# Kernel optimization log

Measured on AMD Instinct MI355X. Metric: run time of the kernel, lower is better.

The kernel has to match this reference:

```python
import jax, jax.numpy as jnp
import numpy as np

D_MODEL = 768
N_HEADS = 12
D_K = D_MODEL // N_HEADS


def setup_inputs() -> dict:
    key = jax.random.key(0)
    k_x, k_wqkv, k_bqkv, k_wo, k_bo = jax.random.split(key, 5)
    s = 1.0 / np.sqrt(D_MODEL)
    return {
        "x": jax.random.normal(k_x, (2, 4096, D_MODEL), dtype=jnp.float32),
        "w_qkv": jax.random.uniform(k_wqkv, (D_MODEL, 3 * D_MODEL), jnp.float32, -s, s),
        "b_qkv": jax.random.uniform(k_bqkv, (3 * D_MODEL,), jnp.float32, -s, s),
        "w_out": jax.random.uniform(k_wo, (D_MODEL, D_MODEL), jnp.float32, -s, s),
        "b_out": jax.random.uniform(k_bo, (D_MODEL,), jnp.float32, -s, s),
    }


def reference(x, w_qkv, b_qkv, w_out, b_out):
    B, S, E = x.shape
    qkv = x @ w_qkv + b_qkv                                  # [B,S,3E]
    qkv = qkv.reshape(B, S, 3, N_HEADS, D_K)
    qkv = jnp.transpose(qkv, (2, 0, 3, 1, 4))                # [3,B,H,S,Dk]
    q, k, v = qkv[0], qkv[1], qkv[2]
    scores = jnp.einsum("bhsd,bhtd->bhst", q, k) / jnp.sqrt(jnp.float32(D_K))
    attn = jax.nn.softmax(scores, axis=-1)                   # [B,H,S,S]
    ctx = jnp.einsum("bhst,bhtd->bhsd", attn, v)             # [B,H,S,Dk]
    ctx = jnp.transpose(ctx, (0, 2, 1, 3)).reshape(B, S, E)  # [B,S,E]
    return ctx @ w_out + b_out
```

## Files before the change

kernel.cpp:

```cpp
#include <hip/hip_runtime.h>

typedef short short8 __attribute__((ext_vector_type(8)));
typedef float f32x4 __attribute__((ext_vector_type(4)));
typedef float f32x16 __attribute__((ext_vector_type(16)));
typedef unsigned short u16;
typedef unsigned int u32;

__device__ __forceinline__ u16 f2bf(float f) {
  u32 u = __float_as_uint(f);
  u32 r = u + 0x7fffu + ((u >> 16) & 1u);
  return (u16)(r >> 16);
}

__device__ __forceinline__ u32 cvtpk(float lo, float hi) {
  u32 r;
  asm("v_cvt_pk_bf16_f32 %0, %1, %2" : "=v"(r) : "v"(lo), "v"(hi));
  return r;
}

__device__ __forceinline__ void async_copy16(u16* lds_dst, const u16* gsrc) {
  __builtin_amdgcn_global_load_lds(
      (const __attribute__((address_space(1))) u32*)gsrc,
      (__attribute__((address_space(3))) u32*)lds_dst, 16, 0, 0);
}

__global__ void cvt_f32_bf16(const float4* __restrict__ in, uint2* __restrict__ out, int n4) {
  int i = blockIdx.x * blockDim.x + threadIdx.x;
  if (i >= n4) return;
  float4 v = in[i];
  uint2 o;
  o.x = (u32)f2bf(v.x) | ((u32)f2bf(v.y) << 16);
  o.y = (u32)f2bf(v.z) | ((u32)f2bf(v.w) << 16);
  out[i] = o;
}

__global__ __launch_bounds__(256) void cvt_transpose_w(
    const float* __restrict__ W, u16* __restrict__ WT, int K, int N) {
  __shared__ float tl[32 * 33];
  int n0 = blockIdx.x * 32, k0 = blockIdx.y * 32;
  int tx = threadIdx.x & 31, ty = threadIdx.x >> 5;
#pragma unroll
  for (int j = 0; j < 4; ++j)
    tl[(ty + j * 8) * 33 + tx] = W[(size_t)(k0 + ty + j * 8) * N + n0 + tx];
  __syncthreads();
#pragma unroll
  for (int j = 0; j < 4; ++j)
    WT[(size_t)(n0 + ty + j * 8) * K + k0 + tx] = f2bf(tl[tx * 33 + ty + j * 8]);
}

__global__ __launch_bounds__(256) void transpose_v(
    const u16* __restrict__ V, u16* __restrict__ VT) {
  __shared__ u16 tb[64 * 66];
  const int tid = threadIdx.x;
  const int bh = blockIdx.y;
  const int t0 = blockIdx.x * 64;
  const u16* Vb = V + (size_t)bh * 4096 * 64;
  u16* VTb = VT + (size_t)bh * 64 * 4096;
#pragma unroll
  for (int it = 0; it < 2; ++it) {
    int cid = it * 256 + tid;
    int row = cid >> 3, c = cid & 7;
    short8 v = *(const short8*)&Vb[(size_t)(t0 + row) * 64 + c * 8];
#pragma unroll
    for (int i = 0; i < 8; ++i) tb[row * 66 + c * 8 + i] = (u16)v[i];
  }
  __syncthreads();
#pragma unroll
  for (int it = 0; it < 2; ++it) {
    int pid = it * 256 + tid;
    int c2 = pid & 7, d = pid >> 3;
    short8 o;
#pragma unroll
    for (int i = 0; i < 8; ++i) o[i] = (short)tb[(c2 * 8 + i) * 66 + d];
    *(short8*)&VTb[(size_t)d * 4096 + t0 + c2 * 8] = o;
  }
}

#define BM 128
#define BN 128
#define BKG 64

template <int EPI>
__global__ __launch_bounds__(256, 2) void gemm_bf16(
    const u16* __restrict__ A, const u16* __restrict__ Bt,
    const float* __restrict__ bias, int M, int N, int K,
    u16* __restrict__ q_out, u16* __restrict__ k_out, u16* __restrict__ v_out,
    float* __restrict__ c_out) {
  __shared__ u16 lA[BM * BKG];
  __shared__ u16 lB[BN * BKG];
  const int tid = threadIdx.x;
  const int lane = tid & 63;
  const int wid = tid >> 6;
  const int r = lane & 15, hi = lane >> 4;
  const int m0 = blockIdx.y * BM;
  const int n0 = blockIdx.x * BN;
  const int wm = (wid >> 1) * 64;
  const int wn = (wid & 1) * 64;

  f32x4 acc[4][4];
#pragma unroll
  for (int i = 0; i < 4; ++i)
#pragma unroll
    for (int j = 0; j < 4; ++j) acc[i][j] = f32x4{0.f, 0.f, 0.f, 0.f};

  for (int k0 = 0; k0 < K; k0 += BKG) {
#pragma unroll
    for (int j = 0; j < 4; ++j) {
      int cid = j * 256 + tid;
      int row = cid >> 3, c = cid & 7;
      async_copy16(&lA[cid * 8], &A[(size_t)(m0 + row) * K + k0 + c * 8]);
    }
#pragma unroll
    for (int j = 0; j < 4; ++j) {
      int cid = j * 256 + tid;
      int row = cid >> 3, c = cid & 7;
      async_copy16(&lB[cid * 8], &Bt[(size_t)(n0 + row) * K + k0 + c * 8]);
    }
    __syncthreads();
#pragma unroll
    for (int kk = 0; kk < 2; ++kk) {
      short8 af[4], bfr[4];
#pragma unroll
      for (int i = 0; i < 4; ++i)
        af[i] = *(const short8*)&lA[(wm + i * 16 + r) * BKG + kk * 32 + hi * 8];
#pragma unroll
      for (int i = 0; i < 4; ++i)
        bfr[i] = *(const short8*)&lB[(wn + i * 16 + r) * BKG + kk * 32 + hi * 8];
#pragma unroll
      for (int i = 0; i < 4; ++i)
#pragma unroll
        for (int j = 0; j < 4; ++j)
          acc[i][j] = __builtin_amdgcn_mfma_f32_16x16x32_bf16(af[i], bfr[j], acc[i][j], 0, 0, 0);
    }
    __syncthreads();
  }

#pragma unroll
  for (int i = 0; i < 4; ++i) {
#pragma unroll
    for (int j = 0; j < 4; ++j) {
      int gn = n0 + wn + j * 16 + r;
      float bv = bias[gn];
#pragma unroll
      for (int q = 0; q < 4; ++q) {
        int gm = m0 + wm + i * 16 + hi * 4 + q;
        float v = acc[i][j][q] + bv;
        if (EPI == 0) {
          int part = gn / 768;
          int rem = gn - part * 768;
          int h = rem >> 6, d = rem & 63;
          int b = gm >> 12, s = gm & 4095;
          size_t off = (((size_t)(b * 12 + h) * 4096) + s) * 64 + d;
          if (part == 0) q_out[off] = f2bf(v * 0.18033688011112042f);
          else if (part == 1) k_out[off] = f2bf(v);
          else v_out[off] = f2bf(v);
        } else {
          c_out[(size_t)gm * N + gn] = v;
        }
      }
    }
  }
}

__global__ __launch_bounds__(256, 3) void attn_fwd(
    const u16* __restrict__ Qg, const u16* __restrict__ Kg,
    const u16* __restrict__ VTg, u16* __restrict__ ctxg) {
  __shared__ u16 lK[2][64 * 64];
  __shared__ u16 lV[2][64 * 64];
  const int tid = threadIdx.x;
  const int lane = tid & 63, wid = tid >> 6;
  const int q32 = lane & 31, half = lane >> 5;
  const int bh = blockIdx.y;
  const int s0 = blockIdx.x * 128;
  const int qrow = s0 + wid * 32 + q32;
  const u16* Qb = Qg + (size_t)bh * 4096 * 64;
  const u16* Kb = Kg + (size_t)bh * 4096 * 64;
  const u16* Vb = VTg + (size_t)bh * 64 * 4096;

  short8 qf[4];
#pragma unroll
  for (int dc = 0; dc < 4; ++dc)
    qf[dc] = *(const short8*)&Qb[(size_t)qrow * 64 + dc * 16 + half * 8];

  f32x16 acc0, acc1;
#pragma unroll
  for (int i = 0; i < 16; ++i) { acc0[i] = 0.f; acc1[i] = 0.f; }
  float l_run = 0.f;

#define STAGE(buf, t0_)                                                      \
  do {                                                                       \
    _Pragma("unroll") for (int j = 0; j < 2; ++j) {                          \
      int cid = j * 256 + tid;                                               \
      int row = cid >> 3, c = cid & 7, cs = c ^ (row & 7);                   \
      async_copy16(&lK[buf][cid * 8], &Kb[(size_t)((t0_) + row) * 64 + cs * 8]); \
    }                                                                        \
    _Pragma("unroll") for (int j = 0; j < 2; ++j) {                          \
      int cid = j * 256 + tid;                                               \
      int row = cid >> 3, c = cid & 7, cs = c ^ (row & 7);                   \
      async_copy16(&lV[buf][cid * 8], &Vb[(size_t)row * 4096 + (t0_) + cs * 8]); \
    }                                                                        \
  } while (0)

  STAGE(0, 0);
  int cur = 0;

  for (int t0 = 0; t0 < 4096; t0 += 64) {
    __syncthreads();
    if (t0 + 64 < 4096) STAGE(cur ^ 1, t0 + 64);

    const char* lKc = (const char*)lK[cur];
    const char* lVc = (const char*)lV[cur];

    f32x16 sA, sB;
#pragma unroll
    for (int i = 0; i < 16; ++i) { sA[i] = 0.f; sB[i] = 0.f; }
    const int xorq = (q32 & 7);
    __builtin_amdgcn_s_setprio(1);
#pragma unroll
    for (int dc = 0; dc < 4; ++dc) {
      int ch = dc * 2 + half;
      short8 kA = *(const short8*)(lKc + q32 * 128 + ((ch ^ xorq) << 4));
      short8 kB = *(const short8*)(lKc + (32 + q32) * 128 + ((ch ^ xorq) << 4));
      sA = __builtin_amdgcn_mfma_f32_32x32x16_bf16(kA, qf[dc], sA, 0, 0, 0);
      sB = __builtin_amdgcn_mfma_f32_32x32x16_bf16(kB, qf[dc], sB, 0, 0, 0);
    }
    __builtin_amdgcn_s_setprio(0);

    float pA[16], pB[16];
#pragma unroll
    for (int i = 0; i < 16; ++i) pA[i] = exp2f(sA[i]);
#pragma unroll
    for (int i = 0; i < 16; ++i) pB[i] = exp2f(sB[i]);
    {
      float ps0 = 0.f, ps1 = 0.f, ps2 = 0.f, ps3 = 0.f;
#pragma unroll
      for (int i = 0; i < 16; i += 4) {
        ps0 += pA[i]; ps1 += pA[i + 1]; ps2 += pA[i + 2]; ps3 += pA[i + 3];
        ps0 += pB[i]; ps1 += pB[i + 1]; ps2 += pB[i + 2]; ps3 += pB[i + 3];
      }
      l_run += (ps0 + ps1) + (ps2 + ps3);
    }

    u32 w0[8], w1[8];
#pragma unroll
    for (int g = 0; g < 4; ++g) {
      w0[g] = cvtpk(pA[4 * g + 0], pA[4 * g + 1]);
      w1[g] = cvtpk(pA[4 * g + 2], pA[4 * g + 3]);
      w0[4 + g] = cvtpk(pB[4 * g + 0], pB[4 * g + 1]);
      w1[4 + g] = cvtpk(pB[4 * g + 2], pB[4 * g + 3]);
    }

    __builtin_amdgcn_s_setprio(1);
#pragma unroll
    for (int ks = 0; ks < 4; ++ks) {
      u32 x0 = w0[2 * ks], y0 = w0[2 * ks + 1];
      u32 x1 = w1[2 * ks], y1 = w1[2 * ks + 1];
      asm("v_permlane32_swap_b32 %0, %1" : "+v"(x0), "+v"(y0));
      asm("v_permlane32_swap_b32 %0, %1" : "+v"(x1), "+v"(y1));
      union { u32 u[4]; short8 s; } pa;
      pa.u[0] = x0; pa.u[1] = x1; pa.u[2] = y0; pa.u[3] = y1;
      int ch = ks * 2 + half;
      {
        int d = q32;
        short8 vf = *(const short8*)(lVc + d * 128 + ((ch ^ (d & 7)) << 4));
        acc0 = __builtin_amdgcn_mfma_f32_32x32x16_bf16(pa.s, vf, acc0, 0, 0, 0);
      }
      {
        int d = 32 + q32;
        short8 vf = *(const short8*)(lVc + d * 128 + ((ch ^ (d & 7)) << 4));
        acc1 = __builtin_amdgcn_mfma_f32_32x32x16_bf16(pa.s, vf, acc1, 0, 0, 0);
      }
    }
    __builtin_amdgcn_s_setprio(0);
    cur ^= 1;
  }

  float l_tot = l_run + __shfl_xor(l_run, 32);
  float inv = 1.f / l_tot;
  int b = bh / 12, h = bh - b * 12;
#pragma unroll
  for (int reg = 0; reg < 16; ++reg) {
    int row = (reg & 3) + 8 * (reg >> 2) + 4 * half;
    float iv = __shfl(inv, row);
    size_t base = ((size_t)b * 4096 + s0 + wid * 32 + row) * 768 + h * 64;
    ctxg[base + q32] = f2bf(acc0[reg] * iv);
    ctxg[base + 32 + q32] = f2bf(acc1[reg] * iv);
  }
}

extern "C" void kernel_launch(void* const* d_in, const int* in_sizes, int n_in,
                              void* d_out, int out_size, void* d_ws, size_t ws_size,
                              hipStream_t stream) {
  const float* x = (const float*)d_in[0];
  const float* w_qkv = (const float*)d_in[1];
  const float* b_qkv = (const float*)d_in[2];
  const float* w_out = (const float*)d_in[3];
  const float* b_out = (const float*)d_in[4];
  float* out = (float*)d_out;

  char* ws = (char*)d_ws;
  const size_t SZ_X = (size_t)8192 * 768 * 2;
  const size_t SZ_WQ = (size_t)2304 * 768 * 2;
  const size_t SZ_WO = (size_t)768 * 768 * 2;
  const size_t SZ_HSD = (size_t)24 * 4096 * 64 * 2;
  u16* xb = (u16*)ws;     ws += SZ_X;
  u16* wqkvT = (u16*)ws;  ws += SZ_WQ;
  u16* woutT = (u16*)ws;  ws += SZ_WO;
  u16* Qb = (u16*)ws;     ws += SZ_HSD;
  u16* Kb = (u16*)ws;     ws += SZ_HSD;
  u16* Vb = (u16*)ws;     ws += SZ_HSD;
  u16* VTb = (u16*)ws;    ws += SZ_HSD;
  u16* ctxb = (u16*)ws;   ws += SZ_X;

  cvt_f32_bf16<<<dim3(6144), dim3(256), 0, stream>>>(
      (const float4*)x, (uint2*)xb, 8192 * 768 / 4);
  cvt_transpose_w<<<dim3(72, 24), dim3(256), 0, stream>>>(w_qkv, wqkvT, 768, 2304);
  cvt_transpose_w<<<dim3(24, 24), dim3(256), 0, stream>>>(w_out, woutT, 768, 768);
  gemm_bf16<0><<<dim3(18, 64), dim3(256), 0, stream>>>(
      xb, wqkvT, b_qkv, 8192, 2304, 768, Qb, Kb, Vb, (float*)nullptr);
  transpose_v<<<dim3(64, 24), dim3(256), 0, stream>>>(Vb, VTb);
  attn_fwd<<<dim3(32, 24), dim3(256), 0, stream>>>(Qb, Kb, VTb, ctxb);
  gemm_bf16<1><<<dim3(6, 64), dim3(256), 0, stream>>>(
      ctxb, woutT, b_out, 8192, 768, 768, (u16*)nullptr, (u16*)nullptr, (u16*)nullptr, out);
}
```

Measured before the change: 255.4 us.

## Software-pipeline attention loop with triple-buffered K/V and QK-ahead overlap

Restructures the attention main loop so each iteration computes the QK scores of the next tile while running softmax and PV on the current tile. K/V go from double to triple buffering in LDS, with prefetch two tiles ahead and the loop unrolled by three so buffer indices are compile-time constants. The first QK MFMA now starts from a zero accumulator instead of zero-filled score registers. The aim is to hide exp/convert latency behind matrix-core work and give loads more time to land. In exchange it uses more LDS per block and keeps more score registers live, which may pressure occupancy.

Result: slower. 452.5 us (+77.2%).

```diff
diff --git a/kernel.cpp b/kernel.cpp
--- a/kernel.cpp
+++ b/kernel.cpp
@@ -165,8 +165,8 @@
 __global__ __launch_bounds__(256, 3) void attn_fwd(
     const u16* __restrict__ Qg, const u16* __restrict__ Kg,
     const u16* __restrict__ VTg, u16* __restrict__ ctxg) {
-  __shared__ u16 lK[2][64 * 64];
-  __shared__ u16 lV[2][64 * 64];
+  __shared__ u16 lK[3][64 * 64];
+  __shared__ u16 lV[3][64 * 64];
   const int tid = threadIdx.x;
   const int lane = tid & 63, wid = tid >> 6;
   const int q32 = lane & 31, half = lane >> 5;
@@ -176,103 +176,126 @@
   const u16* Qb = Qg + (size_t)bh * 4096 * 64;
   const u16* Kb = Kg + (size_t)bh * 4096 * 64;
   const u16* Vb = VTg + (size_t)bh * 64 * 4096;
+  const int xorq = q32 & 7;
 
   short8 qf[4];
 #pragma unroll
   for (int dc = 0; dc < 4; ++dc)
     qf[dc] = *(const short8*)&Qb[(size_t)qrow * 64 + dc * 16 + half * 8];
 
+  f32x16 zc;
+#pragma unroll
+  for (int i = 0; i < 16; ++i) zc[i] = 0.f;
+
   f32x16 acc0, acc1;
 #pragma unroll
   for (int i = 0; i < 16; ++i) { acc0[i] = 0.f; acc1[i] = 0.f; }
   float l_run = 0.f;
-
-#define STAGE(buf, t0_)                                                      \
+  f32x16 sA, sB;
+
+#define STAGE(BUF, TI)                                                       \
   do {                                                                       \
     _Pragma("unroll") for (int j = 0; j < 2; ++j) {                          \
       int cid = j * 256 + tid;                                               \
       int row = cid >> 3, c = cid & 7, cs = c ^ (row & 7);                   \
-      async_copy16(&lK[buf][cid * 8], &Kb[(size_t)((t0_) + row) * 64 + cs * 8]); \
+      async_copy16(&lK[BUF][cid * 8],                                        \
+                   &Kb[(size_t)((TI) * 64 + row) * 64 + cs * 8]);            \
     }                                                                        \
     _Pragma("unroll") for (int j = 0; j < 2; ++j) {                          \
       int cid = j * 256 + tid;                                               \
       int row = cid >> 3, c = cid & 7, cs = c ^ (row & 7);                   \
-      async_copy16(&lV[buf][cid * 8], &Vb[(size_t)row * 4096 + (t0_) + cs * 8]); \
+      async_copy16(&lV[BUF][cid * 8],                                        \
+                   &Vb[(size_t)row * 4096 + (TI) * 64 + cs * 8]);            \
     }                                                                        \
   } while (0)
 
+#define QK_TILE(BUF)                                                          \
+  {                                                                           \
+    const char* lKc = (const char*)lK[BUF];                                   \
+    {                                                                         \
+      short8 kA = *(const short8*)(lKc + q32 * 128 + ((half ^ xorq) << 4));   \
+      short8 kB = *(const short8*)(lKc + (32 + q32) * 128 + ((half ^ xorq) << 4)); \
+      sA = __builtin_amdgcn_mfma_f32_32x32x16_bf16(kA, qf[0], zc, 0, 0, 0);   \
+      sB = __builtin_amdgcn_mfma_f32_32x32x16_bf16(kB, qf[0], zc, 0, 0, 0);   \
+    }                                                                         \
+    _Pragma("unroll") for (int dc = 1; dc < 4; ++dc) {                        \
+      int ch = dc * 2 + half;                                                 \
+      short8 kA = *(const short8*)(lKc + q32 * 128 + ((ch ^ xorq) << 4));     \
+      short8 kB = *(const short8*)(lKc + (32 + q32) * 128 + ((ch ^ xorq) << 4)); \
+      sA = __builtin_amdgcn_mfma_f32_32x32x16_bf16(kA, qf[dc], sA, 0, 0, 0);  \
+      sB = __builtin_amdgcn_mfma_f32_32x32x16_bf16(kB, qf[dc], sB, 0, 0, 0);  \
+    }                                                                         \
+  }
+
+#define SM_TILE()                                                             \
+  u32 w0[8], w1[8];                                                           \
+  {                                                                           \
+    float ps0 = 0.f, ps1 = 0.f, ps2 = 0.f, ps3 = 0.f;                        \
+    _Pragma("unroll") for (int g = 0; g < 4; ++g) {                           \
+      float a0 = exp2f(sA[4 * g + 0]), a1 = exp2f(sA[4 * g + 1]);             \
+      float a2 = exp2f(sA[4 * g + 2]), a3 = exp2f(sA[4 * g + 3]);             \
+      w0[g] = cvtpk(a0, a1); w1[g] = cvtpk(a2, a3);                           \
+      ps0 += a0; ps1 += a1; ps2 += a2; ps3 += a3;                             \
+      float b0 = exp2f(sB[4 * g + 0]), b1 = exp2f(sB[4 * g + 1]);             \
+      float b2 = exp2f(sB[4 * g + 2]), b3 = exp2f(sB[4 * g + 3]);             \
+      w0[4 + g] = cvtpk(b0, b1); w1[4 + g] = cvtpk(b2, b3);                   \
+      ps0 += b0; ps1 += b1; ps2 += b2; ps3 += b3;                             \
+    }                                                                         \
+    l_run += (ps0 + ps1) + (ps2 + ps3);                                       \
+  }
+
+#define PV_TILE(BUF)                                                          \
+  {                                                                           \
+    const char* lVc = (const char*)lV[BUF];                                   \
+    __builtin_amdgcn_s_setprio(1);                                            \
+    _Pragma("unroll") for (int ks = 0; ks < 4; ++ks) {                        \
+      u32 x0 = w0[2 * ks], y0 = w0[2 * ks + 1];                               \
+      u32 x1 = w1[2 * ks], y1 = w1[2 * ks + 1];                               \
+      asm("v_permlane32_swap_b32 %0, %1" : "+v"(x0), "+v"(y0));               \
+      asm("v_permlane32_swap_b32 %0, %1" : "+v"(x1), "+v"(y1));               \
+      union { u32 u[4]; short8 s; } pa;                                       \
+      pa.u[0] = x0; pa.u[1] = x1; pa.u[2] = y0; pa.u[3] = y1;                 \
+      int ch = ks * 2 + half;                                                 \
+      {                                                                       \
+        int d = q32;                                                          \
+        short8 vf = *(const short8*)(lVc + d * 128 + ((ch ^ (d & 7)) << 4));  \
+        acc0 = __builtin_amdgcn_mfma_f32_32x32x16_bf16(pa.s, vf, acc0, 0, 0, 0); \
+      }                                                                       \
+      {                                                                       \
+        int d = 32 + q32;                                                     \
+        short8 vf = *(const short8*)(lVc + d * 128 + ((ch ^ (d & 7)) << 4));  \
+        acc1 = __builtin_amdgcn_mfma_f32_32x32x16_bf16(pa.s, vf, acc1, 0, 0, 0); \
+      }                                                                       \
+    }                                                                         \
+    __builtin_amdgcn_s_setprio(0);                                            \
+  }
+
+#define BODY(B0, B1, B2, T, STG)                                              \
+  {                                                                           \
+    __syncthreads();                                                          \
+    if (STG) STAGE(B2, (T) + 2);                                              \
+    SM_TILE();                                                                \
+    QK_TILE(B1);                                                              \
+    PV_TILE(B0);                                                              \
+  }
+
   STAGE(0, 0);
-  int cur = 0;
-
-  for (int t0 = 0; t0 < 4096; t0 += 64) {
+  STAGE(1, 1);
+  __syncthreads();
+  QK_TILE(0);
+
+  for (int t3 = 0; t3 < 60; t3 += 3) {
+    BODY(0, 1, 2, t3, true);
+    BODY(1, 2, 0, t3 + 1, true);
+    BODY(2, 0, 1, t3 + 2, true);
+  }
+  BODY(0, 1, 2, 60, true);
+  BODY(1, 2, 0, 61, true);
+  BODY(2, 0, 1, 62, false);
+  {
     __syncthreads();
-    if (t0 + 64 < 4096) STAGE(cur ^ 1, t0 + 64);
-
-    const char* lKc = (const char*)lK[cur];
-    const char* lVc = (const char*)lV[cur];
-
-    f32x16 sA, sB;
-#pragma unroll
-    for (int i = 0; i < 16; ++i) { sA[i] = 0.f; sB[i] = 0.f; }
-    const int xorq = (q32 & 7);
-    __builtin_amdgcn_s_setprio(1);
-#pragma unroll
-    for (int dc = 0; dc < 4; ++dc) {
-      int ch = dc * 2 + half;
-      short8 kA = *(const short8*)(lKc + q32 * 128 + ((ch ^ xorq) << 4));
-      short8 kB = *(const short8*)(lKc + (32 + q32) * 128 + ((ch ^ xorq) << 4));
-      sA = __builtin_amdgcn_mfma_f32_32x32x16_bf16(kA, qf[dc], sA, 0, 0, 0);
-      sB = __builtin_amdgcn_mfma_f32_32x32x16_bf16(kB, qf[dc], sB, 0, 0, 0);
-    }
-    __builtin_amdgcn_s_setprio(0);
-
-    float pA[16], pB[16];
-#pragma unroll
-    for (int i = 0; i < 16; ++i) pA[i] = exp2f(sA[i]);
-#pragma unroll
-    for (int i = 0; i < 16; ++i) pB[i] = exp2f(sB[i]);
-    {
-      float ps0 = 0.f, ps1 = 0.f, ps2 = 0.f, ps3 = 0.f;
-#pragma unroll
-      for (int i = 0; i < 16; i += 4) {
-        ps0 += pA[i]; ps1 += pA[i + 1]; ps2 += pA[i + 2]; ps3 += pA[i + 3];
-        ps0 += pB[i]; ps1 += pB[i + 1]; ps2 += pB[i + 2]; ps3 += pB[i + 3];
-      }
-      l_run += (ps0 + ps1) + (ps2 + ps3);
-    }
-
-    u32 w0[8], w1[8];
-#pragma unroll
-    for (int g = 0; g < 4; ++g) {
-      w0[g] = cvtpk(pA[4 * g + 0], pA[4 * g + 1]);
-      w1[g] = cvtpk(pA[4 * g + 2], pA[4 * g + 3]);
-      w0[4 + g] = cvtpk(pB[4 * g + 0], pB[4 * g + 1]);
-      w1[4 + g] = cvtpk(pB[4 * g + 2], pB[4 * g + 3]);
-    }
-
-    __builtin_amdgcn_s_setprio(1);
-#pragma unroll
-    for (int ks = 0; ks < 4; ++ks) {
-      u32 x0 = w0[2 * ks], y0 = w0[2 * ks + 1];
-      u32 x1 = w1[2 * ks], y1 = w1[2 * ks + 1];
-      asm("v_permlane32_swap_b32 %0, %1" : "+v"(x0), "+v"(y0));
-      asm("v_permlane32_swap_b32 %0, %1" : "+v"(x1), "+v"(y1));
-      union { u32 u[4]; short8 s; } pa;
-      pa.u[0] = x0; pa.u[1] = x1; pa.u[2] = y0; pa.u[3] = y1;
-      int ch = ks * 2 + half;
-      {
-        int d = q32;
-        short8 vf = *(const short8*)(lVc + d * 128 + ((ch ^ (d & 7)) << 4));
-        acc0 = __builtin_amdgcn_mfma_f32_32x32x16_bf16(pa.s, vf, acc0, 0, 0, 0);
-      }
-      {
-        int d = 32 + q32;
-        short8 vf = *(const short8*)(lVc + d * 128 + ((ch ^ (d & 7)) << 4));
-        acc1 = __builtin_amdgcn_mfma_f32_32x32x16_bf16(pa.s, vf, acc1, 0, 0, 0);
-      }
-    }
-    __builtin_amdgcn_s_setprio(0);
-    cur ^= 1;
+    SM_TILE();
+    PV_TILE(0);
   }
 
   float l_tot = l_run + __shfl_xor(l_run, 32);
```
